# Kernel tuning notes

Measured on AMD Instinct MI355X. Metric: run time of the kernel, lower is better.

## Reference

```python
import jax, jax.numpy as jnp
import numpy as np

R = 0.2                 # radius (init kwarg r)
MAX_NEIGHBORS = 32      # init kwarg max_num_neighbors
N = 16384
N_BATCH = 8


def setup_inputs() -> dict:
    key = jax.random.key(0)
    k1, k2, k3, k4 = jax.random.split(key, 4)
    node_coord_src = jax.random.uniform(k1, (N, 3), dtype=jnp.float32)
    node_coord_dst = jax.random.uniform(k2, (N, 3), dtype=jnp.float32)
    batch_src = jnp.sort(jax.random.randint(k3, (N,), 0, N_BATCH, dtype=jnp.int64))
    batch_dst = jnp.sort(jax.random.randint(k4, (N,), 0, N_BATCH, dtype=jnp.int64))
    return {
        "node_coord_src": node_coord_src,
        "batch_src": batch_src,
        "node_coord_dst": node_coord_dst,
        "batch_dst": batch_dst,
    }


def reference(node_coord_src, batch_src, node_coord_dst, batch_dst):
    """Batch-aware radius graph: for each dst point, up to MAX_NEIGHBORS src
    points within radius R and in the same batch (deterministically the
    lowest-index ones). Returns fixed-shape padded (edge_src, edge_dst),
    padded with -1 where fewer than MAX_NEIGHBORS neighbors exist."""
    n_src = node_coord_src.shape[0]
    n_dst = node_coord_dst.shape[0]

    # squared pairwise distances [n_dst, n_src] without [N,N,3] intermediate
    s2 = jnp.sum(node_coord_src * node_coord_src, axis=-1)          # [n_src]
    d2 = jnp.sum(node_coord_dst * node_coord_dst, axis=-1)          # [n_dst]
    cross = jnp.einsum("nd,md->nm", node_coord_dst, node_coord_src)  # [n_dst,n_src]
    dist2 = d2[:, None] + s2[None, :] - 2.0 * cross

    valid = (dist2 <= R * R) & (batch_dst[:, None] == batch_src[None, :])

    # pick first MAX_NEIGHBORS valid src indices per dst: encode src index,
    # invalid -> n_src (sentinel), take K smallest via top_k of negation
    src_idx = jnp.arange(n_src, dtype=jnp.int32)
    keyed = jnp.where(valid, src_idx[None, :], n_src)               # [n_dst,n_src]
    neg_sel, _ = jax.lax.top_k(-keyed, MAX_NEIGHBORS)
    sel = -neg_sel                                                  # [n_dst,K]
    found = sel < n_src

    edge_src = jnp.where(found, sel, -1)
    edge_dst = jnp.where(found, jnp.arange(n_dst, dtype=jnp.int32)[:, None], -1)
    return edge_src.reshape(-1), edge_dst.reshape(-1)
```

## Files before the change

### kernel.cpp

```cpp
#include <hip/hip_runtime.h>

#define K 32
#define NB 8
#define MAXM 40

__global__ void bounds_kernel(const int* __restrict__ batch_src, int n_src,
                              int* __restrict__ bounds) {
    const int b = threadIdx.x;
    if (b > NB) return;
    int lo = 0, hi = n_src;
    while (lo < hi) {
        int mid = (lo + hi) >> 1;
        if (batch_src[mid] < b) lo = mid + 1; else hi = mid;
    }
    bounds[b] = lo;
}

__global__ __launch_bounds__(256) void radius_kernel(
    const float* __restrict__ src_xyz,
    const float* __restrict__ dst_xyz, const int* __restrict__ batch_dst,
    const int* __restrict__ bounds, int n_dst, int* __restrict__ out)
{
    __shared__ unsigned long long s_mask[4][MAXM];
    __shared__ int                s_base[4][MAXM];

    const int w    = threadIdx.x >> 6;
    const int lane = threadIdx.x & 63;
    const int d    = (blockIdx.x * blockDim.x + threadIdx.x) >> 6;
    if (d >= n_dst) return;

    const float xd = dst_xyz[3 * d + 0];
    const float yd = dst_xyz[3 * d + 1];
    const float zd = dst_xyz[3 * d + 2];
    const float d2 = __fadd_rn(__fadd_rn(__fmul_rn(xd, xd), __fmul_rn(yd, yd)),
                               __fmul_rn(zd, zd));
    const int b     = batch_dst[d];
    const int start = bounds[b];
    const int end   = bounds[b + 1];

    int count = 0;
    int nm    = 0;

    for (int j0 = start; j0 < end && count < K; j0 += 64) {
        const int j  = j0 + lane;
        const int jc = j < end ? j : end - 1;
        const float xs = src_xyz[3 * jc + 0];
        const float ys = src_xyz[3 * jc + 1];
        const float zs = src_xyz[3 * jc + 2];
        const float s2 = __fadd_rn(
            __fadd_rn(__fmul_rn(xs, xs), __fmul_rn(ys, ys)),
            __fmul_rn(zs, zs));
        const float cross = __fadd_rn(
            __fadd_rn(__fmul_rn(xd, xs), __fmul_rn(yd, ys)),
            __fmul_rn(zd, zs));
        const float dist2 = __fsub_rn(__fadd_rn(d2, s2),
                                      __fmul_rn(2.0f, cross));
        const bool valid = (j < end) && (dist2 <= 0.04f);
        const unsigned long long m = __ballot(valid);
        if (m != 0ull && nm < MAXM) {
            if (lane == 0) { s_mask[w][nm] = m; s_base[w][nm] = j0; }
            count += __popcll(m);
            ++nm;
        }
    }

    const long long obase = (long long)d * K;
    if (lane < K) {
        int rem = lane;
        unsigned long long x = 0ull;
        int jb = 0;
        bool found = false;
        for (int q = 0; q < nm; ++q) {
            const unsigned long long mq = s_mask[w][q];
            const int c = __popcll(mq);
            const bool here = (!found) && (rem < c);
            if (here) { x = mq; jb = s_base[w][q]; }
            if (!found && !here) rem -= c;
            found = found || here;
        }
        int val = -1;
        if (found) {
            int pos = 0;
            unsigned y;
            int c = __popcll(x & 0xFFFFFFFFull);
            if (rem >= c) { rem -= c; y = (unsigned)(x >> 32); pos = 32; }
            else          { y = (unsigned)x; }
            c = __popc(y & 0xFFFFu); if (rem >= c) { rem -= c; y >>= 16; pos += 16; }
            c = __popc(y & 0xFFu);   if (rem >= c) { rem -= c; y >>= 8;  pos += 8;  }
            c = __popc(y & 0xFu);    if (rem >= c) { rem -= c; y >>= 4;  pos += 4;  }
            c = __popc(y & 0x3u);    if (rem >= c) { rem -= c; y >>= 2;  pos += 2;  }
            c = (int)(y & 1u);       if (rem >= c) { pos += 1; }
            val = jb + pos;
        }
        out[obase + lane] = val;
        out[(long long)n_dst * K + obase + lane] = found ? d : -1;
    }
}

extern "C" void kernel_launch(void* const* d_in, const int* in_sizes, int n_in,
                              void* d_out, int out_size, void* d_ws, size_t ws_size,
                              hipStream_t stream) {
    const float* src_xyz   = (const float*)d_in[0];
    const int*   batch_src = (const int*)d_in[1];
    const float* dst_xyz   = (const float*)d_in[2];
    const int*   batch_dst = (const int*)d_in[3];
    int* out    = (int*)d_out;
    int* bounds = (int*)d_ws;

    const int n_src = in_sizes[0] / 3;
    const int n_dst = in_sizes[2] / 3;

    bounds_kernel<<<1, 16, 0, stream>>>(batch_src, n_src, bounds);

    const int threads = 256;
    const int blocks = (n_dst * 64 + threads - 1) / threads;
    radius_kernel<<<blocks, threads, 0, stream>>>(
        src_xyz, dst_xyz, batch_dst, bounds, n_dst, out);
}
```

Measured before the change: 94.36 us.

## Process four dst points per wave with 16-lane groups and prefetched src tiles

Instead of one wavefront scanning 64 src points per step for a single dst point, each wavefront now serves four dst points. Each dst point gets 16 lanes, and one 16-point src tile is shared by all four groups. The next tile's coordinates are loaded one step ahead to hide load latency. The scan ends only when all four groups have found K neighbors or run out of candidates. Selection becomes a per-group prefix-scan compaction through shared memory, and MAXM is raised to hold more ballot masks. The trade-off is that a wave keeps scanning for its slowest group, plus a heavier selection phase and more shared memory per block.

After: 125.3 us. 1.33x slower.

```diff
diff --git a/kernel.cpp b/kernel.cpp
--- a/kernel.cpp
+++ b/kernel.cpp
@@ -2,7 +2,7 @@
 
 #define K 32
 #define NB 8
-#define MAXM 40
+#define MAXM 160
 
 __global__ void bounds_kernel(const int* __restrict__ batch_src, int n_src,
                               int* __restrict__ bounds) {
@@ -19,81 +19,116 @@
 __global__ __launch_bounds__(256) void radius_kernel(
     const float* __restrict__ src_xyz,
     const float* __restrict__ dst_xyz, const int* __restrict__ batch_dst,
-    const int* __restrict__ bounds, int n_dst, int* __restrict__ out)
+    const int* __restrict__ bounds, int n_src, int n_dst,
+    int* __restrict__ out)
 {
     __shared__ unsigned long long s_mask[4][MAXM];
-    __shared__ int                s_base[4][MAXM];
+    __shared__ int                s_tb[4][MAXM];
+    __shared__ int                s_sel[4][4][K];
 
     const int w    = threadIdx.x >> 6;
     const int lane = threadIdx.x & 63;
-    const int d    = (blockIdx.x * blockDim.x + threadIdx.x) >> 6;
-    if (d >= n_dst) return;
+    const int q    = lane >> 4;
+    const int r    = lane & 15;
+    const int wave = (blockIdx.x * blockDim.x + threadIdx.x) >> 6;
+    const int d    = wave * 4 + q;
+    const int dc   = d < n_dst ? d : n_dst - 1;
 
-    const float xd = dst_xyz[3 * d + 0];
-    const float yd = dst_xyz[3 * d + 1];
-    const float zd = dst_xyz[3 * d + 2];
+    const float xd = dst_xyz[3 * dc + 0];
+    const float yd = dst_xyz[3 * dc + 1];
+    const float zd = dst_xyz[3 * dc + 2];
     const float d2 = __fadd_rn(__fadd_rn(__fmul_rn(xd, xd), __fmul_rn(yd, yd)),
                                __fmul_rn(zd, zd));
-    const int b     = batch_dst[d];
-    const int start = bounds[b];
-    const int end   = bounds[b + 1];
+    const int b     = batch_dst[dc];
+    const int my_lo = bounds[b];
+    const int my_hi = bounds[b + 1];
 
+    const int lo_w = __shfl(my_lo, 0);
+    const int hi_w = __shfl(my_hi, 63);
+
+    const unsigned long long qmask = 0xFFFFull << (q * 16);
     int count = 0;
     int nm    = 0;
 
-    for (int j0 = start; j0 < end && count < K; j0 += 64) {
-        const int j  = j0 + lane;
-        const int jc = j < end ? j : end - 1;
-        const float xs = src_xyz[3 * jc + 0];
-        const float ys = src_xyz[3 * jc + 1];
-        const float zs = src_xyz[3 * jc + 2];
-        const float s2 = __fadd_rn(
-            __fadd_rn(__fmul_rn(xs, xs), __fmul_rn(ys, ys)),
-            __fmul_rn(zs, zs));
-        const float cross = __fadd_rn(
-            __fadd_rn(__fmul_rn(xd, xs), __fmul_rn(yd, ys)),
-            __fmul_rn(zd, zs));
-        const float dist2 = __fsub_rn(__fadd_rn(d2, s2),
-                                      __fmul_rn(2.0f, cross));
-        const bool valid = (j < end) && (dist2 <= 0.04f);
-        const unsigned long long m = __ballot(valid);
-        if (m != 0ull && nm < MAXM) {
-            if (lane == 0) { s_mask[w][nm] = m; s_base[w][nm] = j0; }
-            count += __popcll(m);
-            ++nm;
+    if (lo_w < hi_w) {
+        int tile = lo_w;
+        int c  = tile + r;
+        int cc = c < n_src - 1 ? c : n_src - 1;
+        float xs = src_xyz[3 * cc + 0];
+        float ys = src_xyz[3 * cc + 1];
+        float zs = src_xyz[3 * cc + 2];
+        while (true) {
+            const int c2  = tile + 16 + r;
+            const int cc2 = c2 < n_src - 1 ? c2 : n_src - 1;
+            const float xs2 = src_xyz[3 * cc2 + 0];
+            const float ys2 = src_xyz[3 * cc2 + 1];
+            const float zs2 = src_xyz[3 * cc2 + 2];
+
+            const float s2 = __fadd_rn(
+                __fadd_rn(__fmul_rn(xs, xs), __fmul_rn(ys, ys)),
+                __fmul_rn(zs, zs));
+            const float cross = __fadd_rn(
+                __fadd_rn(__fmul_rn(xd, xs), __fmul_rn(yd, ys)),
+                __fmul_rn(zd, zs));
+            const float dist2 = __fsub_rn(__fadd_rn(d2, s2),
+                                          __fmul_rn(2.0f, cross));
+            const bool valid = (c >= my_lo) && (c < my_hi) && (dist2 <= 0.04f);
+            const unsigned long long m = __ballot(valid);
+            if (m != 0ull) {
+                if (lane == 0) { s_mask[w][nm] = m; s_tb[w][nm] = tile; }
+                ++nm;
+                count += (int)__popcll(m & qmask);
+            }
+            const bool fin = (count >= K) || (tile + 16 >= my_hi);
+            tile += 16;
+            if (__all(fin) || tile >= hi_w) break;
+            c = c2; xs = xs2; ys = ys2; zs = zs2;
         }
     }
 
-    const long long obase = (long long)d * K;
-    if (lane < K) {
-        int rem = lane;
-        unsigned long long x = 0ull;
-        int jb = 0;
-        bool found = false;
-        for (int q = 0; q < nm; ++q) {
-            const unsigned long long mq = s_mask[w][q];
-            const int c = __popcll(mq);
-            const bool here = (!found) && (rem < c);
-            if (here) { x = mq; jb = s_base[w][q]; }
-            if (!found && !here) rem -= c;
-            found = found || here;
+    ((int*)s_sel[w])[lane] = -1;
+    ((int*)s_sel[w])[64 + lane] = -1;
+
+    for (int qq = 0; qq < 4; ++qq) {
+        int done = 0;
+        for (int m0 = 0; m0 < nm; m0 += 64) {
+            const int i = m0 + lane;
+            unsigned slice = 0; int tb = 0;
+            if (i < nm) {
+                slice = (unsigned)((s_mask[w][i] >> (qq * 16)) & 0xFFFFull);
+                tb = s_tb[w][i];
+            }
+            const int cpc = __popc(slice);
+            int pref = cpc;
+            #pragma unroll
+            for (int off = 1; off < 64; off <<= 1) {
+                const int t = __shfl_up(pref, off);
+                if (lane >= off) pref += t;
+            }
+            int rank = done + pref - cpc;
+            unsigned x = slice;
+            while (x != 0u && rank < K) {
+                const int t = __ffs(x) - 1;
+                s_sel[w][qq][rank] = tb + t;
+                x &= x - 1;
+                ++rank;
+            }
+            done += __shfl(pref, 63);
+            if (done >= K) break;
         }
-        int val = -1;
-        if (found) {
-            int pos = 0;
-            unsigned y;
-            int c = __popcll(x & 0xFFFFFFFFull);
-            if (rem >= c) { rem -= c; y = (unsigned)(x >> 32); pos = 32; }
-            else          { y = (unsigned)x; }
-            c = __popc(y & 0xFFFFu); if (rem >= c) { rem -= c; y >>= 16; pos += 16; }
-            c = __popc(y & 0xFFu);   if (rem >= c) { rem -= c; y >>= 8;  pos += 8;  }
-            c = __popc(y & 0xFu);    if (rem >= c) { rem -= c; y >>= 4;  pos += 4;  }
-            c = __popc(y & 0x3u);    if (rem >= c) { rem -= c; y >>= 2;  pos += 2;  }
-            c = (int)(y & 1u);       if (rem >= c) { pos += 1; }
-            val = jb + pos;
+    }
+
+    const long long nb = (long long)n_dst * K;
+    #pragma unroll
+    for (int p = 0; p < 2; ++p) {
+        const int idx = p * 64 + lane;
+        const int qq = idx >> 5, k = idx & 31;
+        const int dq = wave * 4 + qq;
+        if (dq < n_dst) {
+            const int val = s_sel[w][qq][k];
+            out[(long long)dq * K + k] = val;
+            out[nb + (long long)dq * K + k] = (val >= 0) ? dq : -1;
         }
-        out[obase + lane] = val;
-        out[(long long)n_dst * K + obase + lane] = found ? d : -1;
     }
 }
 
@@ -112,8 +147,8 @@
 
     bounds_kernel<<<1, 16, 0, stream>>>(batch_src, n_src, bounds);
 
-    const int threads = 256;
-    const int blocks = (n_dst * 64 + threads - 1) / threads;
-    radius_kernel<<<blocks, threads, 0, stream>>>(
-        src_xyz, dst_xyz, batch_dst, bounds, n_dst, out);
+    const int waves  = (n_dst + 3) / 4;
+    const int blocks = (waves + 3) / 4;
+    radius_kernel<<<blocks, 256, 0, stream>>>(
+        src_xyz, dst_xyz, batch_dst, bounds, n_src, n_dst, out);
 }
```
